# Optimization experiments

Hardware: AMD Instinct MI355X
Metric: run time of the kernel (lower is better)

## Reference

```python
import jax, jax.numpy as jnp
import numpy as np

LN_EPS = 1e-5


def _mlp(x, W1, b1, W2, b2, g, beta):
    # build_mlp_d: Linear -> ReLU -> Linear -> LayerNorm (mlp_layers=2, lay_norm=True)
    h = jax.nn.relu(x @ W1 + b1)
    h = h @ W2 + b2
    mu = jnp.mean(h, axis=-1, keepdims=True)
    var = jnp.var(h, axis=-1, keepdims=True)
    return (h - mu) * jax.lax.rsqrt(var + LN_EPS) * g + beta


def setup_inputs() -> dict:
    E, N, L, EIF = 524288, 65536, 128, 3
    key = jax.random.key(0)
    ks = iter(jax.random.split(key, 48))
    def rn(shape, s=1.0):
        return jax.random.normal(next(ks), shape, dtype=jnp.float32) * s
    inp = {}
    inp["edge_index"] = jax.random.randint(next(ks), (2, E), 0, N)
    inp["edge_dx_"] = rn((E, 3))
    inp["edge_attr"] = rn((E, EIF))
    for nm in ["vector_a", "vector_b", "vector_c",
               "senders_v_t_", "senders_v_tm1_", "senders_w_t_", "senders_w_tm1_",
               "senders_a_t_", "senders_alpha_t_",
               "receivers_v_t_", "receivers_v_tm1_", "receivers_w_t_", "receivers_w_tm1_",
               "receivers_a_t_", "receivers_alpha_t_"]:
        inp[nm] = rn((E, 3))
    inp["node_latent"] = rn((N, L))
    def mlp_params(pfx, din):
        inp[pfx + "_W1"] = rn((din, L), 0.05)
        inp[pfx + "_b1"] = jnp.zeros((L,), jnp.float32)
        inp[pfx + "_W2"] = rn((L, L), 0.05)
        inp[pfx + "_b2"] = jnp.zeros((L,), jnp.float32)
        inp[pfx + "_g"] = jnp.ones((L,), jnp.float32)
        inp[pfx + "_beta"] = jnp.zeros((L,), jnp.float32)
    mlp_params("fe", 18)        # edge_feat_encoder
    mlp_params("ee", 1 + EIF)   # edge_encoder
    mlp_params("ie", 3 * L)     # interaction_encoder
    return inp


def reference(edge_index, edge_dx_, edge_attr, vector_a, vector_b, vector_c,
              senders_v_t_, senders_v_tm1_, senders_w_t_, senders_w_tm1_,
              senders_a_t_, senders_alpha_t_,
              receivers_v_t_, receivers_v_tm1_, receivers_w_t_, receivers_w_tm1_,
              receivers_a_t_, receivers_alpha_t_,
              node_latent,
              fe_W1, fe_b1, fe_W2, fe_b2, fe_g, fe_beta,
              ee_W1, ee_b1, ee_W2, ee_b2, ee_g, ee_beta,
              ie_W1, ie_b1, ie_W2, ie_b2, ie_g, ie_beta):
    senders, receivers = edge_index[0], edge_index[1]
    basis = jnp.stack([vector_a, vector_b, vector_c], axis=1)  # [E,3,3]
    # Fuse the 12 small bmm projections into two batched einsums.
    s_stack = jnp.stack([senders_v_t_, senders_v_tm1_, senders_w_t_, senders_w_tm1_,
                         senders_a_t_, senders_alpha_t_], axis=1)   # [E,6,3]
    r_stack = jnp.stack([receivers_v_t_, receivers_v_tm1_, receivers_w_t_, receivers_w_tm1_,
                         receivers_a_t_, receivers_alpha_t_], axis=1)
    s_proj = jnp.einsum('eij,ekj->eki', basis, s_stack)  # [E,6,3]
    r_proj = jnp.einsum('eij,ekj->eki', basis, r_stack)
    # signs: -v_t, -v_tm1, -w_t, +w_tm1, -a_t, +alpha_t (receivers side)
    r_sign = jnp.array([-1.0, -1.0, -1.0, 1.0, -1.0, 1.0], jnp.float32)[None, :, None]
    E = s_proj.shape[0]
    senders_features = s_proj.reshape(E, 18)
    receivers_features = (r_proj * r_sign).reshape(E, 18)
    edge_dx_norm = jnp.linalg.norm(edge_dx_, axis=1, keepdims=True)  # [E,1]
    edge_latent = _mlp(jnp.concatenate([edge_dx_norm, edge_attr], axis=1),
                       ee_W1, ee_b1, ee_W2, ee_b2, ee_g, ee_beta)
    senders_latent = _mlp(senders_features, fe_W1, fe_b1, fe_W2, fe_b2, fe_g, fe_beta)
    receivers_latent = _mlp(receivers_features, fe_W1, fe_b1, fe_W2, fe_b2, fe_g, fe_beta)
    node_sum = node_latent[senders] + node_latent[receivers]  # [E,L]
    msg_input = jnp.concatenate([senders_latent + receivers_latent, node_sum, edge_latent], axis=1)
    return _mlp(msg_input, ie_W1, ie_b1, ie_W2, ie_b2, ie_g, ie_beta)
```

## Files before the change

kernel.cpp:

```cpp
#include <hip/hip_runtime.h>

typedef __attribute__((ext_vector_type(4))) float fx4;
typedef __attribute__((ext_vector_type(8))) unsigned short u16x8;
typedef __attribute__((ext_vector_type(8))) __bf16 bf16x8;

static __device__ __forceinline__ unsigned short f2bf(float f) {
  unsigned int u = __builtin_bit_cast(unsigned int, f);
  u += 0x7fffu + ((u >> 16) & 1u);
  return (unsigned short)(u >> 16);
}
static __device__ __forceinline__ fx4 mfma16(u16x8 a, u16x8 b, fx4 c) {
  return __builtin_amdgcn_mfma_f32_16x16x32_bf16(
      __builtin_bit_cast(bf16x8, a), __builtin_bit_cast(bf16x8, b), c, 0, 0, 0);
}

static __device__ __forceinline__ int swz128(int row, int col) {
  return row * 128 + (col ^ ((row & 7) << 3));
}
static __device__ __forceinline__ int swz32(int row, int col) {
  return row * 32 + (col ^ (((row >> 1) & 3) << 3));
}

#define WT_FE1 0
#define WT_FE2 4096
#define WT_EE1 20480
#define WT_EE2 24576
#define WT_A   40960
#define WT_B   57344
#define WT_C   73728
#define WT_IE2 90112
#define WT_TOTAL 106496

__global__ void prep_weights(const float* __restrict__ feW1, const float* __restrict__ feW2,
                             const float* __restrict__ eeW1, const float* __restrict__ eeW2,
                             const float* __restrict__ ieW1, const float* __restrict__ ieW2,
                             unsigned short* __restrict__ wt) {
  int i = blockIdx.x * 256 + threadIdx.x;
  if (i >= WT_TOTAL) return;
  int base, n, k, kpad;
  float val;
  if (i < WT_FE2)      { base = WT_FE1; n = i >> 5; k = i & 31; kpad = 32;
                         val = (k < 18) ? feW1[k * 128 + n] : 0.f; }
  else if (i < WT_EE1) { base = WT_FE2; int j = i - WT_FE2; n = j >> 7; k = j & 127; kpad = 128;
                         val = feW2[k * 128 + n]; }
  else if (i < WT_EE2) { base = WT_EE1; int j = i - WT_EE1; n = j >> 5; k = j & 31; kpad = 32;
                         val = (k < 4) ? eeW1[k * 128 + n] : 0.f; }
  else if (i < WT_A)   { base = WT_EE2; int j = i - WT_EE2; n = j >> 7; k = j & 127; kpad = 128;
                         val = eeW2[k * 128 + n]; }
  else if (i < WT_B)   { base = WT_A;   int j = i - WT_A;   n = j >> 7; k = j & 127; kpad = 128;
                         val = ieW1[k * 128 + n]; }
  else if (i < WT_C)   { base = WT_B;   int j = i - WT_B;   n = j >> 7; k = j & 127; kpad = 128;
                         val = ieW1[(128 + k) * 128 + n]; }
  else if (i < WT_IE2) { base = WT_C;   int j = i - WT_C;   n = j >> 7; k = j & 127; kpad = 128;
                         val = ieW1[(256 + k) * 128 + n]; }
  else                 { base = WT_IE2; int j = i - WT_IE2; n = j >> 7; k = j & 127; kpad = 128;
                         val = ieW2[k * 128 + n]; }
  int dst = (kpad == 32) ? base + n * 32 + (k ^ (((n >> 1) & 3) << 3))
                         : base + n * 128 + (k ^ ((n & 7) << 3));
  wt[dst] = f2bf(val);
}

template<int KPAD, int KT>
static __device__ __forceinline__ void gemm_lds(const unsigned short* As,
                                                const unsigned short* Ws,
                                                fx4* acc, int l16, int lgr) {
#pragma unroll
  for (int kk = 0; kk < KT; kk++) {
    const int k0 = kk * 32 + lgr * 8;
    u16x8 af = *(const u16x8*)(As + ((KPAD == 32) ? swz32(l16, k0) : swz128(l16, k0)));
#pragma unroll
    for (int nt = 0; nt < 8; nt++) {
      const int n = nt * 16 + l16;
      u16x8 bf = *(const u16x8*)(Ws + ((KPAD == 32) ? swz32(n, k0) : swz128(n, k0)));
      acc[nt] = mfma16(af, bf, acc[nt]);
    }
  }
}

static __device__ __forceinline__ void relu_store(fx4* acc, const float* __restrict__ bias,
                                                  unsigned short* dst, int l16, int lgr) {
#pragma unroll
  for (int nt = 0; nt < 8; nt++) {
    const int col = nt * 16 + l16;
    const float b = bias[col];
#pragma unroll
    for (int r = 0; r < 4; r++) {
      float v = acc[nt][r] + b;
      dst[swz128(lgr * 4 + r, col)] = f2bf(v > 0.f ? v : 0.f);
    }
  }
}

static __device__ __forceinline__ void ln_rows(fx4* acc, const float* __restrict__ bias, int l16) {
  float sum[4] = {0, 0, 0, 0}, sq[4] = {0, 0, 0, 0};
#pragma unroll
  for (int nt = 0; nt < 8; nt++) {
    const float b = bias[nt * 16 + l16];
#pragma unroll
    for (int r = 0; r < 4; r++) {
      float v = acc[nt][r] + b; acc[nt][r] = v;
      sum[r] += v; sq[r] += v * v;
    }
  }
#pragma unroll
  for (int r = 0; r < 4; r++) {
    float s_ = sum[r], q_ = sq[r];
#pragma unroll
    for (int m = 1; m < 16; m <<= 1) { s_ += __shfl_xor(s_, m, 64); q_ += __shfl_xor(q_, m, 64); }
    const float mu = s_ * (1.f / 128.f);
    const float rs = rsqrtf(q_ * (1.f / 128.f) - mu * mu + 1e-5f);
#pragma unroll
    for (int nt = 0; nt < 8; nt++) acc[nt][r] = (acc[nt][r] - mu) * rs;
  }
}

struct ParamsFE {
  const float* basis[3];
  const float* sv[6]; const float* rv[6];
  const float* b1; const float* b2; const float* g; const float* be;
};
struct ParamsEE {
  const float* dx; const float* attr;
  const float* b1; const float* b2; const float* g; const float* be;
};

static __device__ __forceinline__ void fe_body(const ParamsFE& p, unsigned short* lds,
                                               const unsigned short* wt, unsigned short* msg,
                                               int bid, int nblocks, int ntiles) {
  const int tid = threadIdx.x;
  const int wave = tid >> 6, lane = tid & 63;
  const int l16 = lane & 15, lgr = lane >> 4;
#pragma unroll
  for (int i = tid * 8; i < 20480; i += 2048)
    *(u16x8*)(lds + i) = *(const u16x8*)(wt + WT_FE1 + i);
  const unsigned short* W1 = lds;
  const unsigned short* W2 = lds + 4096;
  unsigned short* h1 = lds + 20480 + wave * 5120;
  unsigned short* feat = h1 + 4096;
  __syncthreads();
#pragma unroll
  for (int j = 0; j < 4; j++) {
    int c = 18 + lgr * 4 + j;
    if (c < 32) { feat[swz32(l16, c)] = 0; feat[swz32(16 + l16, c)] = 0; }
  }
  const fx4 z4 = {0.f, 0.f, 0.f, 0.f};

  for (int t = bid; t < ntiles; t += nblocks) {
    const int e0 = t * 64 + wave * 16;
    const size_t e = (size_t)(e0 + l16);
    float bx[3][3];
#pragma unroll
    for (int i = 0; i < 3; i++) {
      const float* bp = p.basis[i] + 3 * e;
      bx[i][0] = bp[0]; bx[i][1] = bp[1]; bx[i][2] = bp[2];
    }
#pragma unroll
    for (int k = 0; k < 6; k++) {
      if ((k & 3) == lgr) {
        const float* vs = p.sv[k] + 3 * e;
        const float* vr = p.rv[k] + 3 * e;
        const float s0 = vs[0], s1 = vs[1], s2 = vs[2];
        const float r0 = vr[0], r1 = vr[1], r2 = vr[2];
        const float sgn = (k != 3 && k != 5) ? -1.f : 1.f;
#pragma unroll
        for (int i = 0; i < 3; i++) {
          feat[swz32(l16, k * 3 + i)] =
              f2bf(bx[i][0] * s0 + bx[i][1] * s1 + bx[i][2] * s2);
          feat[swz32(16 + l16, k * 3 + i)] =
              f2bf((bx[i][0] * r0 + bx[i][1] * r1 + bx[i][2] * r2) * sgn);
        }
      }
    }
    fx4 accA[8], accB[8];
#pragma unroll
    for (int b = 0; b < 8; b++) { accA[b] = z4; accB[b] = z4; }
    {
      const int k0 = lgr * 8;
      u16x8 afA = *(const u16x8*)(feat + swz32(l16, k0));
      u16x8 afB = *(const u16x8*)(feat + swz32(16 + l16, k0));
#pragma unroll
      for (int nt = 0; nt < 8; nt++) {
        u16x8 bf = *(const u16x8*)(W1 + swz32(nt * 16 + l16, k0));
        accA[nt] = mfma16(afA, bf, accA[nt]);
        accB[nt] = mfma16(afB, bf, accB[nt]);
      }
    }
    relu_store(accA, p.b1, h1, l16, lgr);
    relu_store(accB, p.b1, h1 + 2048, l16, lgr);
#pragma unroll
    for (int b = 0; b < 8; b++) { accA[b] = z4; accB[b] = z4; }
#pragma unroll
    for (int c = 0; c < 4; c++) {
      const int k0 = c * 32 + lgr * 8;
      u16x8 afA = *(const u16x8*)(h1 + swz128(l16, k0));
      u16x8 afB = *(const u16x8*)(h1 + 2048 + swz128(l16, k0));
#pragma unroll
      for (int nt = 0; nt < 8; nt++) {
        u16x8 bf = *(const u16x8*)(W2 + swz128(nt * 16 + l16, k0));
        accA[nt] = mfma16(afA, bf, accA[nt]);
        accB[nt] = mfma16(afB, bf, accB[nt]);
      }
    }
    ln_rows(accA, p.b2, l16);
    ln_rows(accB, p.b2, l16);
#pragma unroll
    for (int nt = 0; nt < 8; nt++) {
      const int col = nt * 16 + l16;
      const float gg = p.g[col], bb = p.be[col];
#pragma unroll
      for (int r = 0; r < 4; r++)
        msg[(size_t)(e0 + lgr * 4 + r) * 256 + col] =
            f2bf(accA[nt][r] * gg + bb + accB[nt][r] * gg + bb);
    }
  }
}

static __device__ __forceinline__ void ee_body(const ParamsEE& p, unsigned short* lds,
                                               const unsigned short* wt, unsigned short* msg,
                                               int bid, int nblocks, int ntiles) {
  const int tid = threadIdx.x;
  const int wave = tid >> 6, lane = tid & 63;
  const int l16 = lane & 15, lgr = lane >> 4;
#pragma unroll
  for (int i = tid * 8; i < 20480; i += 2048)
    *(u16x8*)(lds + i) = *(const u16x8*)(wt + WT_EE1 + i);
  const unsigned short* W1 = lds;
  const unsigned short* W2 = lds + 4096;
  unsigned short* h1 = lds + 20480 + wave * 2560;
  unsigned short* feat = h1 + 2048;
  __syncthreads();
#pragma unroll
  for (int j = 0; j < 7; j++) feat[swz32(l16, 4 + lgr * 7 + j)] = 0;
  const fx4 z4 = {0.f, 0.f, 0.f, 0.f};

  for (int t = bid; t < ntiles; t += nblocks) {
    const int e0 = t * 64 + wave * 16;
    const size_t e = (size_t)(e0 + l16);
    if (lgr == 0) {
      float d0 = p.dx[3 * e], d1 = p.dx[3 * e + 1], d2 = p.dx[3 * e + 2];
      feat[swz32(l16, 0)] = f2bf(sqrtf(d0 * d0 + d1 * d1 + d2 * d2));
    } else {
      feat[swz32(l16, lgr)] = f2bf(p.attr[3 * e + (lgr - 1)]);
    }
    fx4 acc[8];
#pragma unroll
    for (int b = 0; b < 8; b++) acc[b] = z4;
    gemm_lds<32, 1>(feat, W1, acc, l16, lgr);
    relu_store(acc, p.b1, h1, l16, lgr);
#pragma unroll
    for (int b = 0; b < 8; b++) acc[b] = z4;
    gemm_lds<128, 4>(h1, W2, acc, l16, lgr);
    ln_rows(acc, p.b2, l16);
#pragma unroll
    for (int nt = 0; nt < 8; nt++) {
      const int col = nt * 16 + l16;
      const float gg = p.g[col], bb = p.be[col];
#pragma unroll
      for (int r = 0; r < 4; r++)
        msg[(size_t)(e0 + lgr * 4 + r) * 256 + 128 + col] =
            f2bf(acc[nt][r] * gg + bb);
    }
  }
}

__global__ __launch_bounds__(256) void feee_kernel(ParamsFE pf, ParamsEE pe,
                                                   const unsigned short* wt,
                                                   unsigned short* msg,
                                                   int nfe, int ntiles) {
  extern __shared__ unsigned short lds[];
  if ((int)blockIdx.x < nfe)
    fe_body(pf, lds, wt, msg, blockIdx.x, nfe, ntiles);
  else
    ee_body(pe, lds, wt, msg, blockIdx.x - nfe, gridDim.x - nfe, ntiles);
}

struct ParamsIE {
  const int* eidx;
  const float* nl;
  const float* b1; const float* b2; const float* g; const float* be;
  const unsigned short* wt;
  const unsigned short* msg;
  float* out;
  int E; int ntiles;
};

__global__ __launch_bounds__(512) void ie_kernel(ParamsIE p) {
  extern __shared__ unsigned short dyn[];
  const int tid = threadIdx.x;
  const int wave = tid >> 6, lane = tid & 63;
  const int l16 = lane & 15, lgr = lane >> 4;
#pragma unroll
  for (int i = tid * 8; i < 49152; i += 4096)
    *(u16x8*)(dyn + i) = *(const u16x8*)(p.wt + WT_A + i);
  const unsigned short* WA = dyn;
  const unsigned short* WB = dyn + 16384;
  const unsigned short* WC = dyn + 32768;
  unsigned short* h1 = dyn + 49152 + wave * 2048;
  __syncthreads();
  const fx4 z4 = {0.f, 0.f, 0.f, 0.f};

  for (int t = blockIdx.x; t < p.ntiles; t += gridDim.x) {
    const int e0 = t * 128 + wave * 16;
    const size_t e = (size_t)(e0 + l16);
    const int sidx = p.eidx[e];
    const int ridx = p.eidx[(size_t)p.E + e];
    const unsigned short* mrow = p.msg + e * 256;
    const float* ns = p.nl + (size_t)sidx * 128;
    const float* nr = p.nl + (size_t)ridx * 128;
    fx4 acc[8];
#pragma unroll
    for (int b = 0; b < 8; b++) acc[b] = z4;
#pragma unroll
    for (int c = 0; c < 4; c++) {
      const int k0 = c * 32 + lgr * 8;
      fx4 a0 = *(const fx4*)(ns + k0), a1 = *(const fx4*)(ns + k0 + 4);
      fx4 b0 = *(const fx4*)(nr + k0), b1 = *(const fx4*)(nr + k0 + 4);
      u16x8 af;
#pragma unroll
      for (int j = 0; j < 4; j++) { af[j] = f2bf(a0[j] + b0[j]); af[4 + j] = f2bf(a1[j] + b1[j]); }
#pragma unroll
      for (int nt = 0; nt < 8; nt++) {
        u16x8 bf = *(const u16x8*)(WB + swz128(nt * 16 + l16, k0));
        acc[nt] = mfma16(af, bf, acc[nt]);
      }
    }
#pragma unroll
    for (int c = 0; c < 4; c++) {
      const int k0 = c * 32 + lgr * 8;
      u16x8 af = *(const u16x8*)(mrow + k0);
#pragma unroll
      for (int nt = 0; nt < 8; nt++) {
        u16x8 bf = *(const u16x8*)(WA + swz128(nt * 16 + l16, k0));
        acc[nt] = mfma16(af, bf, acc[nt]);
      }
    }
#pragma unroll
    for (int c = 0; c < 4; c++) {
      const int k0 = c * 32 + lgr * 8;
      u16x8 af = *(const u16x8*)(mrow + 128 + k0);
#pragma unroll
      for (int nt = 0; nt < 8; nt++) {
        u16x8 bf = *(const u16x8*)(WC + swz128(nt * 16 + l16, k0));
        acc[nt] = mfma16(af, bf, acc[nt]);
      }
    }
    relu_store(acc, p.b1, h1, l16, lgr);
#pragma unroll
    for (int b = 0; b < 8; b++) acc[b] = z4;
    gemm_lds<128, 4>(h1, p.wt + WT_IE2, acc, l16, lgr);
    ln_rows(acc, p.b2, l16);
#pragma unroll
    for (int nt = 0; nt < 8; nt++) {
      const int col = nt * 16 + l16;
      const float gg = p.g[col], bb = p.be[col];
#pragma unroll
      for (int r = 0; r < 4; r++)
        p.out[(size_t)(e0 + lgr * 4 + r) * 128 + col] = acc[nt][r] * gg + bb;
    }
  }
}

extern "C" void kernel_launch(void* const* d_in, const int* in_sizes, int n_in,
                              void* d_out, int out_size, void* d_ws, size_t ws_size,
                              hipStream_t stream) {
  (void)n_in; (void)out_size;
  const int E = in_sizes[1] / 3;
  unsigned short* wt = reinterpret_cast<unsigned short*>(d_ws);
  if (ws_size < (size_t)WT_TOTAL * sizeof(unsigned short)) return;

  prep_weights<<<(WT_TOTAL + 255) / 256, 256, 0, stream>>>(
      (const float*)d_in[19], (const float*)d_in[21],
      (const float*)d_in[25], (const float*)d_in[27],
      (const float*)d_in[31], (const float*)d_in[33], wt);

  unsigned short* msg = (unsigned short*)d_out;

  hipFuncSetAttribute((const void*)feee_kernel,
                      hipFuncAttributeMaxDynamicSharedMemorySize, 81920);
  hipFuncSetAttribute((const void*)ie_kernel,
                      hipFuncAttributeMaxDynamicSharedMemorySize, 131072);

  ParamsFE pf;
  for (int i = 0; i < 3; i++) pf.basis[i] = (const float*)d_in[3 + i];
  for (int k = 0; k < 6; k++) { pf.sv[k] = (const float*)d_in[6 + k]; pf.rv[k] = (const float*)d_in[12 + k]; }
  pf.b1 = (const float*)d_in[20]; pf.b2 = (const float*)d_in[22];
  pf.g  = (const float*)d_in[23]; pf.be = (const float*)d_in[24];

  ParamsEE pe;
  pe.dx = (const float*)d_in[1]; pe.attr = (const float*)d_in[2];
  pe.b1 = (const float*)d_in[26]; pe.b2 = (const float*)d_in[28];
  pe.g  = (const float*)d_in[29]; pe.be = (const float*)d_in[30];

  feee_kernel<<<1536, 256, 81920, stream>>>(pf, pe, wt, msg, 1024, E / 64);

  ParamsIE pi;
  pi.eidx = (const int*)d_in[0];
  pi.nl = (const float*)d_in[18];
  pi.b1 = (const float*)d_in[32]; pi.b2 = (const float*)d_in[34];
  pi.g  = (const float*)d_in[35]; pi.be = (const float*)d_in[36];
  pi.wt = wt; pi.msg = msg; pi.out = (float*)d_out;
  pi.E = E; pi.ntiles = E / 128;
  ie_kernel<<<256, 512, 131072, stream>>>(pi);
}
```

Before: 523.8 us.

## Swap MFMA operands so accumulators hold transposed rows for vectorized epilogues

```diff
diff --git a/kernel.cpp b/kernel.cpp
--- a/kernel.cpp
+++ b/kernel.cpp
@@ -2,6 +2,7 @@
 
 typedef __attribute__((ext_vector_type(4))) float fx4;
 typedef __attribute__((ext_vector_type(8))) unsigned short u16x8;
+typedef __attribute__((ext_vector_type(4))) unsigned short u16x4;
 typedef __attribute__((ext_vector_type(8))) __bf16 bf16x8;
 
 static __device__ __forceinline__ unsigned short f2bf(float f) {
@@ -60,58 +61,43 @@
   wt[dst] = f2bf(val);
 }
 
-template<int KPAD, int KT>
-static __device__ __forceinline__ void gemm_lds(const unsigned short* As,
-                                                const unsigned short* Ws,
-                                                fx4* acc, int l16, int lgr) {
-#pragma unroll
-  for (int kk = 0; kk < KT; kk++) {
-    const int k0 = kk * 32 + lgr * 8;
-    u16x8 af = *(const u16x8*)(As + ((KPAD == 32) ? swz32(l16, k0) : swz128(l16, k0)));
-#pragma unroll
-    for (int nt = 0; nt < 8; nt++) {
-      const int n = nt * 16 + l16;
-      u16x8 bf = *(const u16x8*)(Ws + ((KPAD == 32) ? swz32(n, k0) : swz128(n, k0)));
-      acc[nt] = mfma16(af, bf, acc[nt]);
-    }
-  }
-}
-
-static __device__ __forceinline__ void relu_store(fx4* acc, const float* __restrict__ bias,
-                                                  unsigned short* dst, int l16, int lgr) {
+static __device__ __forceinline__ void relu_store_rm(fx4* acc, const float* __restrict__ bias,
+                                                     unsigned short* h1, int row, int lgr) {
 #pragma unroll
   for (int nt = 0; nt < 8; nt++) {
-    const int col = nt * 16 + l16;
-    const float b = bias[col];
+    const int c0 = nt * 16 + lgr * 4;
+    fx4 b4 = *(const fx4*)(bias + c0);
+    u16x4 o;
 #pragma unroll
     for (int r = 0; r < 4; r++) {
-      float v = acc[nt][r] + b;
-      dst[swz128(lgr * 4 + r, col)] = f2bf(v > 0.f ? v : 0.f);
-    }
-  }
-}
-
-static __device__ __forceinline__ void ln_rows(fx4* acc, const float* __restrict__ bias, int l16) {
-  float sum[4] = {0, 0, 0, 0}, sq[4] = {0, 0, 0, 0};
+      float v = acc[nt][r] + b4[r];
+      o[r] = f2bf(v > 0.f ? v : 0.f);
+    }
+    *(u16x4*)(h1 + swz128(row, c0)) = o;
+  }
+}
+
+static __device__ __forceinline__ void ln_rows_rm(fx4* acc, const float* __restrict__ bias,
+                                                  int lgr) {
+  float s = 0.f, q = 0.f;
 #pragma unroll
   for (int nt = 0; nt < 8; nt++) {
-    const float b = bias[nt * 16 + l16];
+    const int c0 = nt * 16 + lgr * 4;
+    fx4 b4 = *(const fx4*)(bias + c0);
 #pragma unroll
     for (int r = 0; r < 4; r++) {
-      float v = acc[nt][r] + b; acc[nt][r] = v;
-      sum[r] += v; sq[r] += v * v;
-    }
-  }
-#pragma unroll
-  for (int r = 0; r < 4; r++) {
-    float s_ = sum[r], q_ = sq[r];
-#pragma unroll
-    for (int m = 1; m < 16; m <<= 1) { s_ += __shfl_xor(s_, m, 64); q_ += __shfl_xor(q_, m, 64); }
-    const float mu = s_ * (1.f / 128.f);
-    const float rs = rsqrtf(q_ * (1.f / 128.f) - mu * mu + 1e-5f);
-#pragma unroll
-    for (int nt = 0; nt < 8; nt++) acc[nt][r] = (acc[nt][r] - mu) * rs;
-  }
+      float v = acc[nt][r] + b4[r]; acc[nt][r] = v;
+      s += v; q += v * v;
+    }
+  }
+  s += __shfl_xor(s, 16, 64); s += __shfl_xor(s, 32, 64);
+  q += __shfl_xor(q, 16, 64); q += __shfl_xor(q, 32, 64);
+  const float mu = s * (1.f / 128.f);
+  const float rs = rsqrtf(q * (1.f / 128.f) - mu * mu + 1e-5f);
+#pragma unroll
+  for (int nt = 0; nt < 8; nt++)
+#pragma unroll
+    for (int r = 0; r < 4; r++) acc[nt][r] = (acc[nt][r] - mu) * rs;
 }
 
 struct ParamsFE {
@@ -176,41 +162,43 @@
     for (int b = 0; b < 8; b++) { accA[b] = z4; accB[b] = z4; }
     {
       const int k0 = lgr * 8;
-      u16x8 afA = *(const u16x8*)(feat + swz32(l16, k0));
-      u16x8 afB = *(const u16x8*)(feat + swz32(16 + l16, k0));
-#pragma unroll
-      for (int nt = 0; nt < 8; nt++) {
-        u16x8 bf = *(const u16x8*)(W1 + swz32(nt * 16 + l16, k0));
-        accA[nt] = mfma16(afA, bf, accA[nt]);
-        accB[nt] = mfma16(afB, bf, accB[nt]);
-      }
-    }
-    relu_store(accA, p.b1, h1, l16, lgr);
-    relu_store(accB, p.b1, h1 + 2048, l16, lgr);
+      u16x8 xfA = *(const u16x8*)(feat + swz32(l16, k0));
+      u16x8 xfB = *(const u16x8*)(feat + swz32(16 + l16, k0));
+#pragma unroll
+      for (int nt = 0; nt < 8; nt++) {
+        u16x8 wf = *(const u16x8*)(W1 + swz32(nt * 16 + l16, k0));
+        accA[nt] = mfma16(wf, xfA, accA[nt]);
+        accB[nt] = mfma16(wf, xfB, accB[nt]);
+      }
+    }
+    relu_store_rm(accA, p.b1, h1, l16, lgr);
+    relu_store_rm(accB, p.b1, h1, 16 + l16, lgr);
 #pragma unroll
     for (int b = 0; b < 8; b++) { accA[b] = z4; accB[b] = z4; }
 #pragma unroll
     for (int c = 0; c < 4; c++) {
       const int k0 = c * 32 + lgr * 8;
-      u16x8 afA = *(const u16x8*)(h1 + swz128(l16, k0));
-      u16x8 afB = *(const u16x8*)(h1 + 2048 + swz128(l16, k0));
-#pragma unroll
-      for (int nt = 0; nt < 8; nt++) {
-        u16x8 bf = *(const u16x8*)(W2 + swz128(nt * 16 + l16, k0));
-        accA[nt] = mfma16(afA, bf, accA[nt]);
-        accB[nt] = mfma16(afB, bf, accB[nt]);
-      }
-    }
-    ln_rows(accA, p.b2, l16);
-    ln_rows(accB, p.b2, l16);
+      u16x8 xfA = *(const u16x8*)(h1 + swz128(l16, k0));
+      u16x8 xfB = *(const u16x8*)(h1 + swz128(16 + l16, k0));
+#pragma unroll
+      for (int nt = 0; nt < 8; nt++) {
+        u16x8 wf = *(const u16x8*)(W2 + swz128(nt * 16 + l16, k0));
+        accA[nt] = mfma16(wf, xfA, accA[nt]);
+        accB[nt] = mfma16(wf, xfB, accB[nt]);
+      }
+    }
+    ln_rows_rm(accA, p.b2, lgr);
+    ln_rows_rm(accB, p.b2, lgr);
 #pragma unroll
     for (int nt = 0; nt < 8; nt++) {
-      const int col = nt * 16 + l16;
-      const float gg = p.g[col], bb = p.be[col];
+      const int c0 = nt * 16 + lgr * 4;
+      fx4 g4 = *(const fx4*)(p.g + c0);
+      fx4 be4 = *(const fx4*)(p.be + c0);
+      u16x4 o;
 #pragma unroll
       for (int r = 0; r < 4; r++)
-        msg[(size_t)(e0 + lgr * 4 + r) * 256 + col] =
-            f2bf(accA[nt][r] * gg + bb + accB[nt][r] * gg + bb);
+        o[r] = f2bf(accA[nt][r] * g4[r] + be4[r] + accB[nt][r] * g4[r] + be4[r]);
+      *(u16x4*)(msg + (size_t)(e0 + l16) * 256 + c0) = o;
     }
   }
 }
@@ -245,20 +233,38 @@
     fx4 acc[8];
 #pragma unroll
     for (int b = 0; b < 8; b++) acc[b] = z4;
-    gemm_lds<32, 1>(feat, W1, acc, l16, lgr);
-    relu_store(acc, p.b1, h1, l16, lgr);
+    {
+      const int k0 = lgr * 8;
+      u16x8 xf = *(const u16x8*)(feat + swz32(l16, k0));
+#pragma unroll
+      for (int nt = 0; nt < 8; nt++) {
+        u16x8 wf = *(const u16x8*)(W1 + swz32(nt * 16 + l16, k0));
+        acc[nt] = mfma16(wf, xf, acc[nt]);
+      }
+    }
+    relu_store_rm(acc, p.b1, h1, l16, lgr);
 #pragma unroll
     for (int b = 0; b < 8; b++) acc[b] = z4;
-    gemm_lds<128, 4>(h1, W2, acc, l16, lgr);
-    ln_rows(acc, p.b2, l16);
+#pragma unroll
+    for (int c = 0; c < 4; c++) {
+      const int k0 = c * 32 + lgr * 8;
+      u16x8 xf = *(const u16x8*)(h1 + swz128(l16, k0));
+#pragma unroll
+      for (int nt = 0; nt < 8; nt++) {
+        u16x8 wf = *(const u16x8*)(W2 + swz128(nt * 16 + l16, k0));
+        acc[nt] = mfma16(wf, xf, acc[nt]);
+      }
+    }
+    ln_rows_rm(acc, p.b2, lgr);
 #pragma unroll
     for (int nt = 0; nt < 8; nt++) {
-      const int col = nt * 16 + l16;
-      const float gg = p.g[col], bb = p.be[col];
-#pragma unroll
-      for (int r = 0; r < 4; r++)
-        msg[(size_t)(e0 + lgr * 4 + r) * 256 + 128 + col] =
-            f2bf(acc[nt][r] * gg + bb);
+      const int c0 = nt * 16 + lgr * 4;
+      fx4 g4 = *(const fx4*)(p.g + c0);
+      fx4 be4 = *(const fx4*)(p.be + c0);
+      u16x4 o;
+#pragma unroll
+      for (int r = 0; r < 4; r++) o[r] = f2bf(acc[nt][r] * g4[r] + be4[r]);
+      *(u16x4*)(msg + (size_t)(e0 + l16) * 256 + 128 + c0) = o;
     }
   }
 }
@@ -315,47 +321,58 @@
       const int k0 = c * 32 + lgr * 8;
       fx4 a0 = *(const fx4*)(ns + k0), a1 = *(const fx4*)(ns + k0 + 4);
       fx4 b0 = *(const fx4*)(nr + k0), b1 = *(const fx4*)(nr + k0 + 4);
-      u16x8 af;
-#pragma unroll
-      for (int j = 0; j < 4; j++) { af[j] = f2bf(a0[j] + b0[j]); af[4 + j] = f2bf(a1[j] + b1[j]); }
-#pragma unroll
-      for (int nt = 0; nt < 8; nt++) {
-        u16x8 bf = *(const u16x8*)(WB + swz128(nt * 16 + l16, k0));
-        acc[nt] = mfma16(af, bf, acc[nt]);
-      }
-    }
-#pragma unroll
-    for (int c = 0; c < 4; c++) {
-      const int k0 = c * 32 + lgr * 8;
-      u16x8 af = *(const u16x8*)(mrow + k0);
-#pragma unroll
-      for (int nt = 0; nt < 8; nt++) {
-        u16x8 bf = *(const u16x8*)(WA + swz128(nt * 16 + l16, k0));
-        acc[nt] = mfma16(af, bf, acc[nt]);
-      }
-    }
-#pragma unroll
-    for (int c = 0; c < 4; c++) {
-      const int k0 = c * 32 + lgr * 8;
-      u16x8 af = *(const u16x8*)(mrow + 128 + k0);
-#pragma unroll
-      for (int nt = 0; nt < 8; nt++) {
-        u16x8 bf = *(const u16x8*)(WC + swz128(nt * 16 + l16, k0));
-        acc[nt] = mfma16(af, bf, acc[nt]);
-      }
-    }
-    relu_store(acc, p.b1, h1, l16, lgr);
+      u16x8 xf;
+#pragma unroll
+      for (int j = 0; j < 4; j++) { xf[j] = f2bf(a0[j] + b0[j]); xf[4 + j] = f2bf(a1[j] + b1[j]); }
+#pragma unroll
+      for (int nt = 0; nt < 8; nt++) {
+        u16x8 wf = *(const u16x8*)(WB + swz128(nt * 16 + l16, k0));
+        acc[nt] = mfma16(wf, xf, acc[nt]);
+      }
+    }
+#pragma unroll
+    for (int c = 0; c < 4; c++) {
+      const int k0 = c * 32 + lgr * 8;
+      u16x8 xf = *(const u16x8*)(mrow + k0);
+#pragma unroll
+      for (int nt = 0; nt < 8; nt++) {
+        u16x8 wf = *(const u16x8*)(WA + swz128(nt * 16 + l16, k0));
+        acc[nt] = mfma16(wf, xf, acc[nt]);
+      }
+    }
+#pragma unroll
+    for (int c = 0; c < 4; c++) {
+      const int k0 = c * 32 + lgr * 8;
+      u16x8 xf = *(const u16x8*)(mrow + 128 + k0);
+#pragma unroll
+      for (int nt = 0; nt < 8; nt++) {
+        u16x8 wf = *(const u16x8*)(WC + swz128(nt * 16 + l16, k0));
+        acc[nt] = mfma16(wf, xf, acc[nt]);
+      }
+    }
+    relu_store_rm(acc, p.b1, h1, l16, lgr);
 #pragma unroll
     for (int b = 0; b < 8; b++) acc[b] = z4;
-    gemm_lds<128, 4>(h1, p.wt + WT_IE2, acc, l16, lgr);
-    ln_rows(acc, p.b2, l16);
+#pragma unroll
+    for (int c = 0; c < 4; c++) {
+      const int k0 = c * 32 + lgr * 8;
+      u16x8 xf = *(const u16x8*)(h1 + swz128(l16, k0));
+#pragma unroll
+      for (int nt = 0; nt < 8; nt++) {
+        u16x8 wf = *(const u16x8*)(p.wt + WT_IE2 + swz128(nt * 16 + l16, k0));
+        acc[nt] = mfma16(wf, xf, acc[nt]);
+      }
+    }
+    ln_rows_rm(acc, p.b2, lgr);
 #pragma unroll
     for (int nt = 0; nt < 8; nt++) {
-      const int col = nt * 16 + l16;
-      const float gg = p.g[col], bb = p.be[col];
-#pragma unroll
-      for (int r = 0; r < 4; r++)
-        p.out[(size_t)(e0 + lgr * 4 + r) * 128 + col] = acc[nt][r] * gg + bb;
+      const int c0 = nt * 16 + lgr * 4;
+      fx4 g4 = *(const fx4*)(p.g + c0);
+      fx4 be4 = *(const fx4*)(p.be + c0);
+      fx4 o;
+#pragma unroll
+      for (int r = 0; r < 4; r++) o[r] = acc[nt][r] * g4[r] + be4[r];
+      *(fx4*)(p.out + (size_t)(e0 + l16) * 128 + c0) = o;
     }
   }
 }
```

Measured after the change: 640.3 us. 22.2% more time.
